# Performance work log

Hardware: AMD Instinct MI355X
Metric: run time of the kernel (lower is better)

The kernel has to match this reference:

```python
import jax, jax.numpy as jnp
import numpy as np

WINDOW = (2, 6, 12)  # (Wz, Wy, Wx)
HEADS = 6


def _position_index(window):
    Wz, Wy, Wx = window
    cz, cy, cx = np.arange(Wz), np.arange(Wy), np.arange(Wx)
    coords = np.stack(np.meshgrid(cz, cy, cx, indexing='ij'))  # [3, Wz, Wy, Wx]
    cf = coords.reshape(3, -1)                                  # [3, N]
    rel = cf[:, :, None] - cf[:, None, :]                       # [3, N, N]
    rel = rel.transpose(1, 2, 0).astype(np.int64)               # [N, N, 3]
    rel[:, :, 0] += Wz - 1
    rel[:, :, 1] += Wy - 1
    rel[:, :, 2] += Wx - 1
    rel[:, :, 0] *= 2 * Wy - 1
    return jnp.asarray(rel.sum(-1).reshape(-1))                 # [N*N]


def setup_inputs() -> dict:
    key = jax.random.key(0)
    ks = jax.random.split(key, 7)
    dim, N, B_, nW = 192, 144, 1024, 512
    table_rows = (2 * WINDOW[2] - 1) * (2 * WINDOW[1] - 1) * (2 * WINDOW[0] - 1)  # 759
    return {
        'x': jax.random.normal(ks[0], (B_, N, dim), jnp.float32),
        'mask': jax.random.normal(ks[1], (nW, N, N), jnp.float32),
        'w_qkv': jax.random.normal(ks[2], (dim, 3 * dim), jnp.float32) * 0.02,
        'b_qkv': jax.random.normal(ks[3], (3 * dim,), jnp.float32) * 0.02,
        'w_o': jax.random.normal(ks[4], (dim, dim), jnp.float32) * 0.02,
        'b_o': jax.random.normal(ks[5], (dim,), jnp.float32) * 0.02,
        'bias_table': jax.random.normal(ks[6], (table_rows, 1, HEADS), jnp.float32) * 0.02,
    }


def reference(x, mask, w_qkv, b_qkv, w_o, b_o, bias_table):
    B_, N, dim = x.shape
    H = HEADS
    hd = dim // H
    scale = hd ** -0.5

    qkv = x @ w_qkv + b_qkv                              # [B_, N, 3*dim]
    qkv = qkv.reshape(B_, N, 3, H, hd).transpose(2, 0, 3, 1, 4)
    q, k, v = qkv[0], qkv[1], qkv[2]                     # [B_, H, N, hd]

    attn = jnp.einsum('bhnd,bhmd->bhnm', q * scale, k)   # [B_, H, N, N]

    pos_idx = _position_index(WINDOW)                    # [N*N] int constant
    bias = bias_table[pos_idx].reshape(N, N, H).transpose(2, 0, 1)  # [H, N, N]
    attn = attn + bias[None]

    nW = mask.shape[0]
    attn = attn.reshape(B_ // nW, nW, H, N, N) + mask[None, :, None]
    attn = jax.nn.softmax(attn.reshape(B_, H, N, N), axis=-1)

    out = jnp.einsum('bhnm,bhmd->bhnd', attn, v)         # [B_, H, N, hd]
    out = out.transpose(0, 2, 1, 3).reshape(B_, N, dim)
    return out @ w_o + b_o
```

## Files before the change

### kernel.cpp

```cpp
#include <hip/hip_runtime.h>

typedef __attribute__((ext_vector_type(4))) float  f32x4;
typedef __attribute__((ext_vector_type(4))) float  float4v;
typedef __attribute__((ext_vector_type(4))) short  short4v;
typedef __attribute__((ext_vector_type(8))) short  short8v;
typedef __attribute__((ext_vector_type(8))) __bf16 bf16x8;

union Frag { short4v h[2]; short8v s8; };

__device__ __forceinline__ short f2bf(float f) {
  unsigned u = __builtin_bit_cast(unsigned, f);
  u = (u + 0x7fffu + ((u >> 16) & 1u)) >> 16;
  return (short)u;
}

__device__ __forceinline__ f32x4 mfma_bf16(const Frag& a, const Frag& b, f32x4 c) {
  return __builtin_amdgcn_mfma_f32_16x16x32_bf16(
      __builtin_bit_cast(bf16x8, a.s8), __builtin_bit_cast(bf16x8, b.s8), c, 0, 0, 0);
}

__device__ __forceinline__ int poscode(int i) {
  int z = (i >= 72) ? 1 : 0;
  int rem = i - 72 * z;
  int y = rem / 12;
  return 11 * z + y + (rem - 12 * y);
}

__global__ __launch_bounds__(256) void k_transpose_w(
    const float* __restrict__ w_qkv, const float* __restrict__ w_o,
    short* __restrict__ wtq, short* __restrict__ wto) {
  int idx = blockIdx.x * 256 + threadIdx.x;
  if (idx < 110592) {
    int k = idx / 576, c = idx % 576;
    wtq[c * 192 + k] = f2bf(w_qkv[idx]);
  } else {
    int j = idx - 110592;
    int k = j / 192, c = j % 192;
    wto[c * 192 + k] = f2bf(w_o[j]);
  }
}

__global__ __launch_bounds__(256, 2) void k_qkv(
    const float* __restrict__ x, const float* __restrict__ bqkv,
    const short* __restrict__ wtq, short* __restrict__ qkv) {
  __shared__ short a_lds[64][200];
  __shared__ short bT[576][40];
  const int tid = threadIdx.x;
  const int lane = tid & 63, wv = tid >> 6;
  const int l15 = lane & 15, lg = lane >> 4;
  const int row0 = blockIdx.x * 64;

#pragma unroll
  for (int i = 0; i < 12; ++i) {
    int flat = tid + 256 * i;
    int r = flat / 48, c4 = flat % 48;
    float4v xv = *(const float4v*)&x[(size_t)(row0 + r) * 192 + c4 * 4];
    short4v sv = { f2bf(xv[0]), f2bf(xv[1]), f2bf(xv[2]), f2bf(xv[3]) };
    *(short4v*)&a_lds[r][c4 * 4] = sv;
  }

  f32x4 acc[36];
#pragma unroll
  for (int i = 0; i < 36; ++i) acc[i] = f32x4{0.f, 0.f, 0.f, 0.f};

  for (int kc = 0; kc < 6; ++kc) {
    __syncthreads();
#pragma unroll
    for (int i = 0; i < 18; ++i) {
      int flat = tid + 256 * i;
      int c = flat >> 3, kk = (flat & 7) << 2;
      *(short4v*)&bT[c][kk] = *(const short4v*)&wtq[c * 192 + kc * 32 + kk];
    }
    __syncthreads();
    Frag a;
    a.h[0] = *(const short4v*)&a_lds[wv * 16 + l15][kc * 32 + lg * 4];
    a.h[1] = *(const short4v*)&a_lds[wv * 16 + l15][kc * 32 + lg * 4 + 16];
#pragma unroll
    for (int cf = 0; cf < 36; ++cf) {
      Frag bw;
      bw.h[0] = *(const short4v*)&bT[cf * 16 + l15][lg * 4];
      bw.h[1] = *(const short4v*)&bT[cf * 16 + l15][lg * 4 + 16];
      acc[cf] = mfma_bf16(a, bw, acc[cf]);
    }
  }

#pragma unroll
  for (int cf = 0; cf < 36; ++cf) {
    int c = cf * 16 + l15;
    int part = c / 192, rem = c % 192;
    int h = rem >> 5, d = rem & 31;
    float bias = bqkv[c];
    float scale = (part == 0) ? 0.17677669529663687f : 1.0f;
#pragma unroll
    for (int r = 0; r < 4; ++r) {
      int g = row0 + wv * 16 + lg * 4 + r;
      int b_ = g / 144, n = g - b_ * 144;
      float v = (acc[cf][r] + bias) * scale;
      qkv[(size_t)((part * 1024 + b_) * 6 + h) * 4608 + n * 32 + d] = f2bf(v);
    }
  }
}

__global__ __launch_bounds__(512, 2) void k_attn(
    const short* __restrict__ qkv, const float* __restrict__ mask,
    const float* __restrict__ btab, float* __restrict__ out) {
  __shared__ short k_l[6][144][40];
  __shared__ short vt[6][32][152];
  const int tid = threadIdx.x;
  const int lane = tid & 63, wv = tid >> 6;
  const int l15 = lane & 15, lg = lane >> 4;

  const int bid = blockIdx.x;
  const int b = ((bid >> 4) << 3) + (bid & 7) + (((bid >> 3) & 1) << 9);
  const int wm = b & 511;

  const size_t kbase = (size_t)(1024 + b) * 6 * 4608;
#pragma unroll
  for (int i = 0; i < 7; ++i) {
    int flat = tid + 512 * i;
    if (flat < 3456) {
      int h = flat / 576, r = flat % 576;
      int n = r >> 2, d8 = (r & 3) * 8;
      *(short8v*)&k_l[h][n][d8] =
          *(const short8v*)&qkv[kbase + (size_t)h * 4608 + n * 32 + d8];
    }
  }
  const size_t vbase = (size_t)(2048 + b) * 6 * 4608;
#pragma unroll
  for (int i = 0; i < 14; ++i) {
    int flat = tid + 512 * i;
    if (flat < 6912) {
      int h = flat / 1152, r = flat % 1152;
      int n = r >> 3, d4 = (r & 7) * 4;
      short4v vv = *(const short4v*)&qkv[vbase + (size_t)h * 4608 + n * 32 + d4];
      vt[h][d4 + 0][n] = vv[0];
      vt[h][d4 + 1][n] = vv[1];
      vt[h][d4 + 2][n] = vv[2];
      vt[h][d4 + 3][n] = vv[3];
    }
  }
  __syncthreads();

  int cnb6[9];
#pragma unroll
  for (int cf = 0; cf < 9; ++cf) cnb6[cf] = 6 * poscode(cf * 16 + lg * 4);
  const float* maskw = &mask[(size_t)wm * 20736];
  const size_t qb = (size_t)b * 6 * 4608;

  f32x4 mrow[9];
  int C0 = 0, q = 0;
  for (int unit = 0; unit < 7; ++unit) {
    int t, h;
    if (unit < 6) { t = wv; h = unit; }
    else { if (wv >= 6) break; t = 8; h = wv; }
    if (unit == 0 || unit == 6) {
      q = t * 16 + l15;
#pragma unroll
      for (int cf = 0; cf < 9; ++cf)
        mrow[cf] = *(const float4v*)&maskw[q * 144 + cf * 16 + lg * 4];
      C0 = (poscode(q) + 27) * 6;
    }

    const short* qrow = &qkv[qb + (size_t)h * 4608 + q * 32];
    Frag aq;
    aq.h[0] = *(const short4v*)&qrow[lg * 4];
    aq.h[1] = *(const short4v*)&qrow[lg * 4 + 16];

    f32x4 s[9];
#pragma unroll
    for (int cf = 0; cf < 9; ++cf) {
      Frag bk;
      bk.h[0] = *(const short4v*)&k_l[h][cf * 16 + l15][lg * 4];
      bk.h[1] = *(const short4v*)&k_l[h][cf * 16 + l15][lg * 4 + 16];
      s[cf] = mfma_bf16(bk, aq, f32x4{0.f, 0.f, 0.f, 0.f});
    }
#pragma unroll
    for (int cf = 0; cf < 9; ++cf) {
      const int i0 = C0 + h - cnb6[cf];
#pragma unroll
      for (int reg = 0; reg < 4; ++reg)
        s[cf][reg] += mrow[cf][reg] + btab[i0 - 6 * reg];
    }

    float mx = s[0][0];
#pragma unroll
    for (int cf = 0; cf < 9; ++cf)
#pragma unroll
      for (int reg = 0; reg < 4; ++reg) mx = fmaxf(mx, s[cf][reg]);
    mx = fmaxf(mx, __shfl_xor(mx, 16, 64));
    mx = fmaxf(mx, __shfl_xor(mx, 32, 64));
    float sum = 0.f;
#pragma unroll
    for (int cf = 0; cf < 9; ++cf)
#pragma unroll
      for (int reg = 0; reg < 4; ++reg) {
        float e = __expf(s[cf][reg] - mx);
        s[cf][reg] = e;
        sum += e;
      }
    sum += __shfl_xor(sum, 16, 64);
    sum += __shfl_xor(sum, 32, 64);
    const float rinv = 1.0f / sum;
#pragma unroll
    for (int cf = 0; cf < 9; ++cf)
#pragma unroll
      for (int reg = 0; reg < 4; ++reg) s[cf][reg] *= rinv;

    f32x4 o0 = {0.f, 0.f, 0.f, 0.f}, o1 = {0.f, 0.f, 0.f, 0.f};
#pragma unroll
    for (int kc = 0; kc < 5; ++kc) {
      Frag ap, b0, b1;
      ap.h[0] = short4v{ f2bf(s[2 * kc][0]), f2bf(s[2 * kc][1]),
                         f2bf(s[2 * kc][2]), f2bf(s[2 * kc][3]) };
      b0.h[0] = *(const short4v*)&vt[h][l15][kc * 32 + lg * 4];
      b1.h[0] = *(const short4v*)&vt[h][16 + l15][kc * 32 + lg * 4];
      if (kc < 4) {
        ap.h[1] = short4v{ f2bf(s[2 * kc + 1][0]), f2bf(s[2 * kc + 1][1]),
                           f2bf(s[2 * kc + 1][2]), f2bf(s[2 * kc + 1][3]) };
        b0.h[1] = *(const short4v*)&vt[h][l15][kc * 32 + lg * 4 + 16];
        b1.h[1] = *(const short4v*)&vt[h][16 + l15][kc * 32 + lg * 4 + 16];
      } else {
        ap.h[1] = short4v{0, 0, 0, 0};
        b0.h[1] = short4v{0, 0, 0, 0};
        b1.h[1] = short4v{0, 0, 0, 0};
      }
      o0 = mfma_bf16(ap, b0, o0);
      o1 = mfma_bf16(ap, b1, o1);
    }
#pragma unroll
    for (int rr = 0; rr < 4; ++rr) {
      const int m = t * 16 + lg * 4 + rr;
      const size_t base = (size_t)(b * 144 + m) * 192 + h * 32;
      out[base + l15]      = o0[rr];
      out[base + 16 + l15] = o1[rr];
    }
  }
}

__global__ __launch_bounds__(256, 2) void k_oproj(
    float* __restrict__ io, const float* __restrict__ bo,
    const short* __restrict__ wto) {
  __shared__ short a_lds[64][200];
  __shared__ short bT[192][40];
  const int tid = threadIdx.x;
  const int lane = tid & 63, wv = tid >> 6;
  const int l15 = lane & 15, lg = lane >> 4;
  const int row0 = blockIdx.x * 64;

#pragma unroll
  for (int i = 0; i < 12; ++i) {
    int flat = tid + 256 * i;
    int r = flat / 48, c4 = flat % 48;
    float4v xv = *(const float4v*)&io[(size_t)(row0 + r) * 192 + c4 * 4];
    short4v sv = { f2bf(xv[0]), f2bf(xv[1]), f2bf(xv[2]), f2bf(xv[3]) };
    *(short4v*)&a_lds[r][c4 * 4] = sv;
  }

  f32x4 acc[12];
#pragma unroll
  for (int i = 0; i < 12; ++i) acc[i] = f32x4{0.f, 0.f, 0.f, 0.f};

  for (int kc = 0; kc < 6; ++kc) {
    __syncthreads();
#pragma unroll
    for (int i = 0; i < 6; ++i) {
      int flat = tid + 256 * i;
      int c = flat >> 3, kk = (flat & 7) << 2;
      *(short4v*)&bT[c][kk] = *(const short4v*)&wto[c * 192 + kc * 32 + kk];
    }
    __syncthreads();
    Frag a;
    a.h[0] = *(const short4v*)&a_lds[wv * 16 + l15][kc * 32 + lg * 4];
    a.h[1] = *(const short4v*)&a_lds[wv * 16 + l15][kc * 32 + lg * 4 + 16];
#pragma unroll
    for (int cf = 0; cf < 12; ++cf) {
      Frag bw;
      bw.h[0] = *(const short4v*)&bT[cf * 16 + l15][lg * 4];
      bw.h[1] = *(const short4v*)&bT[cf * 16 + l15][lg * 4 + 16];
      acc[cf] = mfma_bf16(a, bw, acc[cf]);
    }
  }

#pragma unroll
  for (int cf = 0; cf < 12; ++cf) {
    int c = cf * 16 + l15;
    float bias = bo[c];
#pragma unroll
    for (int r = 0; r < 4; ++r) {
      int g = row0 + wv * 16 + lg * 4 + r;
      io[(size_t)g * 192 + c] = acc[cf][r] + bias;
    }
  }
}

extern "C" void kernel_launch(void* const* d_in, const int* in_sizes, int n_in,
                              void* d_out, int out_size, void* d_ws, size_t ws_size,
                              hipStream_t stream) {
  const float* x    = (const float*)d_in[0];
  const float* mask = (const float*)d_in[1];
  const float* wqkv = (const float*)d_in[2];
  const float* bqkv = (const float*)d_in[3];
  const float* wo   = (const float*)d_in[4];
  const float* bo   = (const float*)d_in[5];
  const float* btab = (const float*)d_in[6];
  float* out = (float*)d_out;

  short* wtq = (short*)d_ws;
  short* wto = wtq + 110592;
  short* qkv = wto + 36864;

  k_transpose_w<<<576, 256, 0, stream>>>(wqkv, wo, wtq, wto);
  k_qkv<<<2304, 256, 0, stream>>>(x, bqkv, wtq, qkv);
  k_attn<<<1024, 512, 0, stream>>>(qkv, mask, btab, out);
  k_oproj<<<2304, 256, 0, stream>>>(out, bo, wto);
}
```

Measured before the change: 320.5 us.

## Permute K dimension for 128-bit fragment loads and precompute dense bias

```diff
diff --git a/kernel.cpp b/kernel.cpp
--- a/kernel.cpp
+++ b/kernel.cpp
@@ -24,6 +24,10 @@
   int rem = i - 72 * z;
   int y = rem / 12;
   return 11 * z + y + (rem - 12 * y);
+}
+
+__device__ __forceinline__ int kperm(int r) {
+  return (r & 16) ? (((r - 16) >> 2) * 8 + 4 + (r & 3)) : ((r >> 2) * 8 + (r & 3));
 }
 
 __global__ __launch_bounds__(256) void k_transpose_w(
@@ -32,12 +36,21 @@
   int idx = blockIdx.x * 256 + threadIdx.x;
   if (idx < 110592) {
     int k = idx / 576, c = idx % 576;
-    wtq[c * 192 + k] = f2bf(w_qkv[idx]);
+    int kp = (k & ~31) + kperm(k & 31);
+    wtq[c * 192 + kp] = f2bf(w_qkv[idx]);
   } else {
     int j = idx - 110592;
     int k = j / 192, c = j % 192;
     wto[c * 192 + k] = f2bf(w_o[j]);
   }
+}
+
+__global__ __launch_bounds__(256) void k_bias(
+    const float* __restrict__ btab, float* __restrict__ bias6) {
+  int idx = blockIdx.x * 256 + threadIdx.x;
+  if (idx >= 124416) return;
+  int h = idx / 20736, r = idx % 20736, m = r / 144, n = r % 144;
+  bias6[idx] = btab[(poscode(m) - poscode(n) + 27) * 6 + h];
 }
 
 __global__ __launch_bounds__(256, 2) void k_qkv(
@@ -56,7 +69,9 @@
     int r = flat / 48, c4 = flat % 48;
     float4v xv = *(const float4v*)&x[(size_t)(row0 + r) * 192 + c4 * 4];
     short4v sv = { f2bf(xv[0]), f2bf(xv[1]), f2bf(xv[2]), f2bf(xv[3]) };
-    *(short4v*)&a_lds[r][c4 * 4] = sv;
+    int k = c4 * 4, rr = k & 31;
+    int pos = (k & ~31) + ((rr & 16) ? (((rr - 16) >> 2) * 8 + 4) : ((rr >> 2) * 8));
+    *(short4v*)&a_lds[r][pos] = sv;
   }
 
   f32x4 acc[36];
@@ -66,20 +81,18 @@
   for (int kc = 0; kc < 6; ++kc) {
     __syncthreads();
 #pragma unroll
-    for (int i = 0; i < 18; ++i) {
+    for (int i = 0; i < 9; ++i) {
       int flat = tid + 256 * i;
-      int c = flat >> 3, kk = (flat & 7) << 2;
-      *(short4v*)&bT[c][kk] = *(const short4v*)&wtq[c * 192 + kc * 32 + kk];
+      int c = flat >> 2, j = flat & 3;
+      *(short8v*)&bT[c][j * 8] = *(const short8v*)&wtq[c * 192 + kc * 32 + j * 8];
     }
     __syncthreads();
     Frag a;
-    a.h[0] = *(const short4v*)&a_lds[wv * 16 + l15][kc * 32 + lg * 4];
-    a.h[1] = *(const short4v*)&a_lds[wv * 16 + l15][kc * 32 + lg * 4 + 16];
+    a.s8 = *(const short8v*)&a_lds[wv * 16 + l15][kc * 32 + lg * 8];
 #pragma unroll
     for (int cf = 0; cf < 36; ++cf) {
       Frag bw;
-      bw.h[0] = *(const short4v*)&bT[cf * 16 + l15][lg * 4];
-      bw.h[1] = *(const short4v*)&bT[cf * 16 + l15][lg * 4 + 16];
+      bw.s8 = *(const short8v*)&bT[cf * 16 + l15][lg * 8];
       acc[cf] = mfma_bf16(a, bw, acc[cf]);
     }
   }
@@ -89,6 +102,7 @@
     int c = cf * 16 + l15;
     int part = c / 192, rem = c % 192;
     int h = rem >> 5, d = rem & 31;
+    int dd = (part == 2) ? d : kperm(d);
     float bias = bqkv[c];
     float scale = (part == 0) ? 0.17677669529663687f : 1.0f;
 #pragma unroll
@@ -96,16 +110,16 @@
       int g = row0 + wv * 16 + lg * 4 + r;
       int b_ = g / 144, n = g - b_ * 144;
       float v = (acc[cf][r] + bias) * scale;
-      qkv[(size_t)((part * 1024 + b_) * 6 + h) * 4608 + n * 32 + d] = f2bf(v);
+      qkv[(size_t)((part * 1024 + b_) * 6 + h) * 4608 + n * 32 + dd] = f2bf(v);
     }
   }
 }
 
 __global__ __launch_bounds__(512, 2) void k_attn(
     const short* __restrict__ qkv, const float* __restrict__ mask,
-    const float* __restrict__ btab, float* __restrict__ out) {
+    const float* __restrict__ bias6, float* __restrict__ out) {
   __shared__ short k_l[6][144][40];
-  __shared__ short vt[6][32][152];
+  __shared__ short vt[6][32][168];
   const int tid = threadIdx.x;
   const int lane = tid & 63, wv = tid >> 6;
   const int l15 = lane & 15, lg = lane >> 4;
@@ -120,10 +134,17 @@
     int flat = tid + 512 * i;
     if (flat < 3456) {
       int h = flat / 576, r = flat % 576;
-      int n = r >> 2, d8 = (r & 3) * 8;
-      *(short8v*)&k_l[h][n][d8] =
-          *(const short8v*)&qkv[kbase + (size_t)h * 4608 + n * 32 + d8];
-    }
+      int n = r >> 2, j8 = (r & 3) * 8;
+      *(short8v*)&k_l[h][n][j8] =
+          *(const short8v*)&qkv[kbase + (size_t)h * 4608 + n * 32 + j8];
+    }
+  }
+#pragma unroll
+  for (int i = 0; i < 6; ++i) {
+    int flat = tid + 512 * i;
+    int h = flat / 512, r = flat & 511;
+    int d = r >> 4, jj = r & 15;
+    vt[h][d][128 + (jj >> 2) * 8 + 4 + (jj & 3)] = 0;
   }
   const size_t vbase = (size_t)(2048 + b) * 6 * 4608;
 #pragma unroll
@@ -133,22 +154,20 @@
       int h = flat / 1152, r = flat % 1152;
       int n = r >> 3, d4 = (r & 7) * 4;
       short4v vv = *(const short4v*)&qkv[vbase + (size_t)h * 4608 + n * 32 + d4];
-      vt[h][d4 + 0][n] = vv[0];
-      vt[h][d4 + 1][n] = vv[1];
-      vt[h][d4 + 2][n] = vv[2];
-      vt[h][d4 + 3][n] = vv[3];
+      int np = (n & ~31) + kperm(n & 31);
+      vt[h][d4 + 0][np] = vv[0];
+      vt[h][d4 + 1][np] = vv[1];
+      vt[h][d4 + 2][np] = vv[2];
+      vt[h][d4 + 3][np] = vv[3];
     }
   }
   __syncthreads();
 
-  int cnb6[9];
-#pragma unroll
-  for (int cf = 0; cf < 9; ++cf) cnb6[cf] = 6 * poscode(cf * 16 + lg * 4);
   const float* maskw = &mask[(size_t)wm * 20736];
   const size_t qb = (size_t)b * 6 * 4608;
 
   f32x4 mrow[9];
-  int C0 = 0, q = 0;
+  int q = 0;
   for (int unit = 0; unit < 7; ++unit) {
     int t, h;
     if (unit < 6) { t = wv; h = unit; }
@@ -158,28 +177,23 @@
 #pragma unroll
       for (int cf = 0; cf < 9; ++cf)
         mrow[cf] = *(const float4v*)&maskw[q * 144 + cf * 16 + lg * 4];
-      C0 = (poscode(q) + 27) * 6;
-    }
-
-    const short* qrow = &qkv[qb + (size_t)h * 4608 + q * 32];
+    }
+
     Frag aq;
-    aq.h[0] = *(const short4v*)&qrow[lg * 4];
-    aq.h[1] = *(const short4v*)&qrow[lg * 4 + 16];
+    aq.s8 = *(const short8v*)&qkv[qb + (size_t)h * 4608 + q * 32 + lg * 8];
 
     f32x4 s[9];
 #pragma unroll
     for (int cf = 0; cf < 9; ++cf) {
       Frag bk;
-      bk.h[0] = *(const short4v*)&k_l[h][cf * 16 + l15][lg * 4];
-      bk.h[1] = *(const short4v*)&k_l[h][cf * 16 + l15][lg * 4 + 16];
+      bk.s8 = *(const short8v*)&k_l[h][cf * 16 + l15][lg * 8];
       s[cf] = mfma_bf16(bk, aq, f32x4{0.f, 0.f, 0.f, 0.f});
     }
+    const float* brow = &bias6[(size_t)(h * 144 + q) * 144];
 #pragma unroll
     for (int cf = 0; cf < 9; ++cf) {
-      const int i0 = C0 + h - cnb6[cf];
-#pragma unroll
-      for (int reg = 0; reg < 4; ++reg)
-        s[cf][reg] += mrow[cf][reg] + btab[i0 - 6 * reg];
+      float4v bv = *(const float4v*)&brow[cf * 16 + lg * 4];
+      s[cf] += mrow[cf] + bv;
     }
 
     float mx = s[0][0];
@@ -212,18 +226,12 @@
       Frag ap, b0, b1;
       ap.h[0] = short4v{ f2bf(s[2 * kc][0]), f2bf(s[2 * kc][1]),
                          f2bf(s[2 * kc][2]), f2bf(s[2 * kc][3]) };
-      b0.h[0] = *(const short4v*)&vt[h][l15][kc * 32 + lg * 4];
-      b1.h[0] = *(const short4v*)&vt[h][16 + l15][kc * 32 + lg * 4];
-      if (kc < 4) {
-        ap.h[1] = short4v{ f2bf(s[2 * kc + 1][0]), f2bf(s[2 * kc + 1][1]),
-                           f2bf(s[2 * kc + 1][2]), f2bf(s[2 * kc + 1][3]) };
-        b0.h[1] = *(const short4v*)&vt[h][l15][kc * 32 + lg * 4 + 16];
-        b1.h[1] = *(const short4v*)&vt[h][16 + l15][kc * 32 + lg * 4 + 16];
-      } else {
-        ap.h[1] = short4v{0, 0, 0, 0};
-        b0.h[1] = short4v{0, 0, 0, 0};
-        b1.h[1] = short4v{0, 0, 0, 0};
-      }
+      ap.h[1] = (kc < 4)
+          ? short4v{ f2bf(s[2 * kc + 1][0]), f2bf(s[2 * kc + 1][1]),
+                     f2bf(s[2 * kc + 1][2]), f2bf(s[2 * kc + 1][3]) }
+          : short4v{0, 0, 0, 0};
+      b0.s8 = *(const short8v*)&vt[h][l15][kc * 32 + lg * 8];
+      b1.s8 = *(const short8v*)&vt[h][16 + l15][kc * 32 + lg * 8];
       o0 = mfma_bf16(ap, b0, o0);
       o1 = mfma_bf16(ap, b1, o1);
     }
@@ -305,12 +313,14 @@
   const float* btab = (const float*)d_in[6];
   float* out = (float*)d_out;
 
-  short* wtq = (short*)d_ws;
-  short* wto = wtq + 110592;
-  short* qkv = wto + 36864;
+  short* wtq   = (short*)d_ws;
+  short* wto   = wtq + 110592;
+  short* qkv   = wto + 36864;
+  float* bias6 = (float*)(qkv + 84934656);
 
   k_transpose_w<<<576, 256, 0, stream>>>(wqkv, wo, wtq, wto);
+  k_bias<<<486, 256, 0, stream>>>(btab, bias6);
   k_qkv<<<2304, 256, 0, stream>>>(x, bqkv, wtq, qkv);
-  k_attn<<<1024, 512, 0, stream>>>(qkv, mask, btab, out);
+  k_attn<<<1024, 512, 0, stream>>>(qkv, mask, bias6, out);
   k_oproj<<<2304, 256, 0, stream>>>(out, bo, wto);
 }
```

Result: faster. 267.8 us (-16.5%).
